# Performance work log

Measured on AMD Instinct MI355X. Metric: run time of the kernel, lower is better.

## Reference

```python
import jax, jax.numpy as jnp
import numpy as np

B, A, F, C = 32, 64, 128, 128


def _mlp(h, W0, b0, W1, b1):
    # LinearLayer stack: Linear(2F->C) + ReLU, Linear(C->C) + ReLU
    h = jax.nn.relu(h @ W0 + b0)
    h = jax.nn.relu(h @ W1 + b1)
    return h


def setup_inputs() -> dict:
    key = jax.random.key(0)
    k0, k1, k2 = jax.random.split(key, 3)
    x = jax.random.normal(k0, (B, A, F), dtype=jnp.float32)
    W0 = jax.random.normal(k1, (2 * F, C), dtype=jnp.float32) * (1.0 / np.sqrt(2 * F))
    b0 = jnp.zeros((C,), dtype=jnp.float32)
    W1 = jax.random.normal(k2, (C, C), dtype=jnp.float32) * (1.0 / np.sqrt(C))
    b1 = jnp.zeros((C,), dtype=jnp.float32)
    return {"x": x, "W0": W0, "b0": b0, "W1": W1, "b1": b1}


def reference(x, W0, b0, W1, b1):
    nb, na, nf = x.shape
    # atom_tile[b,i,j]   = x[b,i]  (first atom of the pair)
    # atom_repeat[b,i,j] = x[b,j]  (second atom of the pair)
    xi = jnp.broadcast_to(x[:, :, None, :], (nb, na, na, nf))
    xj = jnp.broadcast_to(x[:, None, :, :], (nb, na, na, nf))
    # pair_x0 = cat(atom_tile, atom_repeat) = [x_i, x_j]
    p0 = jnp.concatenate([xi, xj], axis=-1).reshape(nb * na * na, 2 * nf)
    # pair_x1 = cat(atom_repeat, atom_tile) = [x_j, x_i]
    p1 = jnp.concatenate([xj, xi], axis=-1).reshape(nb * na * na, 2 * nf)
    h0 = _mlp(p0, W0, b0, W1, b1).reshape(nb, na * na, -1)
    h1 = _mlp(p1, W0, b0, W1, b1).reshape(nb, na * na, -1)
    return h0 + h1
```

## Files before the change

kernel.cpp:

```cpp
#include <hip/hip_runtime.h>
#include <hip/hip_bf16.h>

typedef float  f32x4  __attribute__((ext_vector_type(4)));
typedef __bf16 bf16x8 __attribute__((ext_vector_type(8)));
typedef unsigned int   u32x4 __attribute__((ext_vector_type(4)));
typedef unsigned short u16x4 __attribute__((ext_vector_type(4)));

#define NB 32
#define NA 64
#define NF 128
#define NC 128

__global__ __launch_bounds__(512) void prep_kernel(
    const float* __restrict__ x, const float* __restrict__ W0,
    const float* __restrict__ b0, const float* __restrict__ W1,
    float* __restrict__ u, float* __restrict__ v,
    unsigned short* __restrict__ w1t)
{
    int blk = blockIdx.x;
    int tid = threadIdx.x;
    if (blk < 256) {
        __shared__ __align__(16) float xs[8 * 128];
        int b = blk >> 3;
        int g = blk & 7;
        if (tid < 256)
            ((f32x4*)xs)[tid] =
                ((const f32x4*)(x + (size_t)(b * NA + g * 8) * NF))[tid];
        __syncthreads();
        int c = tid & 127;
        int h = (tid >> 7) & 1;
        int s = tid >> 8;
        const float* wp = W0 + (size_t)h * 128 * NC + c;
        const float* xp = xs + s * 4 * 128;
        float a0 = 0.f, a1 = 0.f, a2 = 0.f, a3 = 0.f;
        #pragma unroll 8
        for (int f = 0; f < 128; ++f) {
            float w = wp[(size_t)f * NC];
            a0 = fmaf(xp[f],       w, a0);
            a1 = fmaf(xp[128 + f], w, a1);
            a2 = fmaf(xp[256 + f], w, a2);
            a3 = fmaf(xp[384 + f], w, a3);
        }
        int row = b * NA + g * 8 + s * 4;
        if (h == 0) {
            u[(size_t)(row + 0) * NC + c] = a0;
            u[(size_t)(row + 1) * NC + c] = a1;
            u[(size_t)(row + 2) * NC + c] = a2;
            u[(size_t)(row + 3) * NC + c] = a3;
        } else {
            float bb = b0[c];
            v[(size_t)(row + 0) * NC + c] = a0 + bb;
            v[(size_t)(row + 1) * NC + c] = a1 + bb;
            v[(size_t)(row + 2) * NC + c] = a2 + bb;
            v[(size_t)(row + 3) * NC + c] = a3 + bb;
        }
    } else {
        int t = (blk - 256) * 512 + tid;
        int n = t >> 5;
        int k = (t & 31) * 4;
        u16x4 o;
        #pragma unroll
        for (int e = 0; e < 4; ++e) {
            float w = W1[(size_t)(k + e) * NC + n];
            o[e] = __builtin_bit_cast(unsigned short, (__bf16)w);
        }
        *(u16x4*)(w1t + (size_t)n * NC + k) = o;
    }
}

__device__ inline bf16x8 relu_cvt_bf16(f32x4 a, f32x4 b)
{
    bf16x8 r;
    #pragma unroll
    for (int e = 0; e < 4; ++e) {
        r[e]     = (__bf16)fmaxf(a[e], 0.f);
        r[e + 4] = (__bf16)fmaxf(b[e], 0.f);
    }
    return r;
}

__global__ __launch_bounds__(256, 3) void pair_mlp_kernel(
    const float* __restrict__ b1g, const float* __restrict__ u,
    const float* __restrict__ v, const unsigned short* __restrict__ w1t,
    float* __restrict__ out)
{
    __shared__ __align__(16) float          u_s[16 * 128];
    __shared__ __align__(16) float          v_s[16 * 128];
    __shared__ __align__(16) unsigned short w_s[128 * 128];

    int blk = blockIdx.x;
    int b = blk / 36;
    int t = blk % 36;
    int I = 0;
    while (t >= 8 - I) { t -= 8 - I; ++I; }
    int J = I + t;

    int tid = threadIdx.x;

    #pragma unroll
    for (int p = 0; p < 4; ++p) {
        int idx = p * 256 + tid;
        int arr = idx >> 9;
        int rem = idx & 511;
        int row = rem >> 5;
        int c   = rem & 31;
        int ga  = b * NA + ((row < 8) ? (I * 8 + row) : (J * 8 + (row & 7)));
        const float* src = (arr ? v : u) + (size_t)ga * NC;
        float*       dst = (arr ? v_s : u_s) + row * 128;
        int sc = (c & 24) | ((c ^ row) & 7);
        ((f32x4*)dst)[sc] = ((const f32x4*)src)[c];
    }
    #pragma unroll
    for (int p = 0; p < 8; ++p) {
        int idx = p * 256 + tid;
        int n = idx >> 4;
        int c = idx & 15;
        int sc = c ^ (n & 7);
        ((u32x4*)(w_s + n * 128))[sc] = ((const u32x4*)(w1t + (size_t)n * NC))[c];
    }
    __syncthreads();

    int wave = tid >> 6;
    int lane = tid & 63;
    int llo  = lane & 15;
    int lhi  = lane >> 4;
    int r    = wave * 16 + llo;
    int il   = r >> 3;
    int jl   = r & 7;

    f32x4 acc0[8], acc1[8];
    f32x4 z = {0.f, 0.f, 0.f, 0.f};
    #pragma unroll
    for (int nf = 0; nf < 8; ++nf) { acc0[nf] = z; acc1[nf] = z; }

    const float* uI = u_s + il * 128;
    const float* vI = v_s + il * 128;
    const float* uJ = u_s + (8 + jl) * 128;
    const float* vJ = v_s + (8 + jl) * 128;

    #pragma unroll
    for (int kk = 0; kk < 4; ++kk) {
        int kc  = kk * 8 + lhi * 2;
        int kc1 = kc + 1;
        int sA0 = (kc  & 24) | ((kc  ^ il) & 7);
        int sA1 = (kc1 & 24) | ((kc1 ^ il) & 7);
        int sB0 = (kc  & 24) | ((kc  ^ jl) & 7);
        int sB1 = (kc1 & 24) | ((kc1 ^ jl) & 7);

        f32x4 uIa = ((const f32x4*)uI)[sA0];
        f32x4 uIb = ((const f32x4*)uI)[sA1];
        f32x4 vIa = ((const f32x4*)vI)[sA0];
        f32x4 vIb = ((const f32x4*)vI)[sA1];
        f32x4 uJa = ((const f32x4*)uJ)[sB0];
        f32x4 uJb = ((const f32x4*)uJ)[sB1];
        f32x4 vJa = ((const f32x4*)vJ)[sB0];
        f32x4 vJb = ((const f32x4*)vJ)[sB1];

        bf16x8 h0 = relu_cvt_bf16(uIa + vJa, uIb + vJb);
        bf16x8 h1 = relu_cvt_bf16(uJa + vIa, uJb + vIb);

        int kcw = kk * 4 + lhi;
        int scW = kcw ^ (llo & 7);
        #pragma unroll
        for (int nf = 0; nf < 8; ++nf) {
            bf16x8 wf = ((const bf16x8*)(w_s + (nf * 16 + llo) * 128))[scW];
            acc0[nf] = __builtin_amdgcn_mfma_f32_16x16x32_bf16(wf, h0, acc0[nf], 0, 0, 0);
            acc1[nf] = __builtin_amdgcn_mfma_f32_16x16x32_bf16(wf, h1, acc1[nf], 0, 0, 0);
        }
    }

    int Ig = I * 8 + il;
    int Jg = J * 8 + jl;
    float* p1 = out + ((size_t)b * 4096 + Ig * 64 + Jg) * 128 + lhi * 4;
    float* p2 = out + ((size_t)b * 4096 + Jg * 64 + Ig) * 128 + lhi * 4;
    bool mirror = (I != J);
    #pragma unroll
    for (int nf = 0; nf < 8; ++nf) {
        f32x4 bias = *(const f32x4*)(b1g + nf * 16 + lhi * 4);
        f32x4 val;
        #pragma unroll
        for (int e = 0; e < 4; ++e)
            val[e] = fmaxf(acc0[nf][e] + bias[e], 0.f) +
                     fmaxf(acc1[nf][e] + bias[e], 0.f);
        *(f32x4*)(p1 + nf * 16) = val;
        if (mirror)
            *(f32x4*)(p2 + nf * 16) = val;
    }
}

extern "C" void kernel_launch(void* const* d_in, const int* in_sizes, int n_in,
                              void* d_out, int out_size, void* d_ws, size_t ws_size,
                              hipStream_t stream)
{
    (void)in_sizes; (void)n_in; (void)out_size; (void)ws_size;
    const float* x  = (const float*)d_in[0];
    const float* W0 = (const float*)d_in[1];
    const float* b0 = (const float*)d_in[2];
    const float* W1 = (const float*)d_in[3];
    const float* b1 = (const float*)d_in[4];
    float* out = (float*)d_out;

    float* u = (float*)d_ws;
    float* v = u + (size_t)NB * NA * NC;
    unsigned short* w1t = (unsigned short*)(v + (size_t)NB * NA * NC);

    prep_kernel<<<264, 512, 0, stream>>>(x, W0, b0, W1, u, v, w1t);
    pair_mlp_kernel<<<32 * 36, 256, 0, stream>>>(b1, u, v, w1t, out);
}
```

Baseline: 31.56 us.

## Pre-pack W1 into MFMA fragment order and load it directly from global memory

After: 43.99 us. +39.4%, slower.

```diff
diff --git a/kernel.cpp b/kernel.cpp
--- a/kernel.cpp
+++ b/kernel.cpp
@@ -15,7 +15,7 @@
     const float* __restrict__ x, const float* __restrict__ W0,
     const float* __restrict__ b0, const float* __restrict__ W1,
     float* __restrict__ u, float* __restrict__ v,
-    unsigned short* __restrict__ w1t)
+    unsigned short* __restrict__ wfrag)
 {
     int blk = blockIdx.x;
     int tid = threadIdx.x;
@@ -55,16 +55,23 @@
             v[(size_t)(row + 3) * NC + c] = a3 + bb;
         }
     } else {
-        int t = (blk - 256) * 512 + tid;
-        int n = t >> 5;
-        int k = (t & 31) * 4;
+        int idx  = ((blk - 256) * 512 + tid) * 4;
+        int e0   = idx & 7;
+        int lane = (idx >> 3) & 63;
+        int frag = idx >> 9;
+        int kk   = frag >> 3;
+        int nf   = frag & 7;
+        int llo  = lane & 15;
+        int lhi  = lane >> 4;
+        int n    = nf * 16 + llo;
+        int kb   = kk * 32 + lhi * 8 + e0;
         u16x4 o;
         #pragma unroll
         for (int e = 0; e < 4; ++e) {
-            float w = W1[(size_t)(k + e) * NC + n];
+            float w = W1[(size_t)(kb + e) * NC + n];
             o[e] = __builtin_bit_cast(unsigned short, (__bf16)w);
         }
-        *(u16x4*)(w1t + (size_t)n * NC + k) = o;
+        *(u16x4*)(wfrag + idx) = o;
     }
 }
 
@@ -79,14 +86,13 @@
     return r;
 }
 
-__global__ __launch_bounds__(256, 3) void pair_mlp_kernel(
+__global__ __launch_bounds__(256, 4) void pair_mlp_kernel(
     const float* __restrict__ b1g, const float* __restrict__ u,
-    const float* __restrict__ v, const unsigned short* __restrict__ w1t,
+    const float* __restrict__ v, const unsigned short* __restrict__ wfrag,
     float* __restrict__ out)
 {
-    __shared__ __align__(16) float          u_s[16 * 128];
-    __shared__ __align__(16) float          v_s[16 * 128];
-    __shared__ __align__(16) unsigned short w_s[128 * 128];
+    __shared__ __align__(16) float u_s[16 * 128];
+    __shared__ __align__(16) float v_s[16 * 128];
 
     int blk = blockIdx.x;
     int b = blk / 36;
@@ -110,14 +116,6 @@
         int sc = (c & 24) | ((c ^ row) & 7);
         ((f32x4*)dst)[sc] = ((const f32x4*)src)[c];
     }
-    #pragma unroll
-    for (int p = 0; p < 8; ++p) {
-        int idx = p * 256 + tid;
-        int n = idx >> 4;
-        int c = idx & 15;
-        int sc = c ^ (n & 7);
-        ((u32x4*)(w_s + n * 128))[sc] = ((const u32x4*)(w1t + (size_t)n * NC))[c];
-    }
     __syncthreads();
 
     int wave = tid >> 6;
@@ -137,6 +135,7 @@
     const float* vI = v_s + il * 128;
     const float* uJ = u_s + (8 + jl) * 128;
     const float* vJ = v_s + (8 + jl) * 128;
+    const bf16x8* wf = (const bf16x8*)wfrag;
 
     #pragma unroll
     for (int kk = 0; kk < 4; ++kk) {
@@ -159,13 +158,11 @@
         bf16x8 h0 = relu_cvt_bf16(uIa + vJa, uIb + vJb);
         bf16x8 h1 = relu_cvt_bf16(uJa + vIa, uJb + vIb);
 
-        int kcw = kk * 4 + lhi;
-        int scW = kcw ^ (llo & 7);
         #pragma unroll
         for (int nf = 0; nf < 8; ++nf) {
-            bf16x8 wf = ((const bf16x8*)(w_s + (nf * 16 + llo) * 128))[scW];
-            acc0[nf] = __builtin_amdgcn_mfma_f32_16x16x32_bf16(wf, h0, acc0[nf], 0, 0, 0);
-            acc1[nf] = __builtin_amdgcn_mfma_f32_16x16x32_bf16(wf, h1, acc1[nf], 0, 0, 0);
+            bf16x8 w = wf[(kk * 8 + nf) * 64 + lane];
+            acc0[nf] = __builtin_amdgcn_mfma_f32_16x16x32_bf16(w, h0, acc0[nf], 0, 0, 0);
+            acc1[nf] = __builtin_amdgcn_mfma_f32_16x16x32_bf16(w, h1, acc1[nf], 0, 0, 0);
         }
     }
 
@@ -202,8 +199,8 @@
 
     float* u = (float*)d_ws;
     float* v = u + (size_t)NB * NA * NC;
-    unsigned short* w1t = (unsigned short*)(v + (size_t)NB * NA * NC);
-
-    prep_kernel<<<264, 512, 0, stream>>>(x, W0, b0, W1, u, v, w1t);
-    pair_mlp_kernel<<<32 * 36, 256, 0, stream>>>(b1, u, v, w1t, out);
-}
+    unsigned short* wfrag = (unsigned short*)(v + (size_t)NB * NA * NC);
+
+    prep_kernel<<<264, 512, 0, stream>>>(x, W0, b0, W1, u, v, wfrag);
+    pair_mlp_kernel<<<32 * 36, 256, 0, stream>>>(b1, u, v, wfrag, out);
+}
```

## Fuse first-layer projection into pair MLP kernel with register-resident W1 fragments

Applied to the files above, without the earlier changes.

After: 34.96 us. +10.8%, slower.

```diff
diff --git a/kernel.cpp b/kernel.cpp
--- a/kernel.cpp
+++ b/kernel.cpp
@@ -12,60 +12,44 @@
 #define NC 128
 
 __global__ __launch_bounds__(512) void prep_kernel(
-    const float* __restrict__ x, const float* __restrict__ W0,
-    const float* __restrict__ b0, const float* __restrict__ W1,
-    float* __restrict__ u, float* __restrict__ v,
-    unsigned short* __restrict__ w1t)
-{
-    int blk = blockIdx.x;
-    int tid = threadIdx.x;
-    if (blk < 256) {
-        __shared__ __align__(16) float xs[8 * 128];
-        int b = blk >> 3;
-        int g = blk & 7;
-        if (tid < 256)
-            ((f32x4*)xs)[tid] =
-                ((const f32x4*)(x + (size_t)(b * NA + g * 8) * NF))[tid];
-        __syncthreads();
-        int c = tid & 127;
-        int h = (tid >> 7) & 1;
-        int s = tid >> 8;
-        const float* wp = W0 + (size_t)h * 128 * NC + c;
-        const float* xp = xs + s * 4 * 128;
-        float a0 = 0.f, a1 = 0.f, a2 = 0.f, a3 = 0.f;
-        #pragma unroll 8
-        for (int f = 0; f < 128; ++f) {
-            float w = wp[(size_t)f * NC];
-            a0 = fmaf(xp[f],       w, a0);
-            a1 = fmaf(xp[128 + f], w, a1);
-            a2 = fmaf(xp[256 + f], w, a2);
-            a3 = fmaf(xp[384 + f], w, a3);
-        }
-        int row = b * NA + g * 8 + s * 4;
-        if (h == 0) {
-            u[(size_t)(row + 0) * NC + c] = a0;
-            u[(size_t)(row + 1) * NC + c] = a1;
-            u[(size_t)(row + 2) * NC + c] = a2;
-            u[(size_t)(row + 3) * NC + c] = a3;
-        } else {
-            float bb = b0[c];
-            v[(size_t)(row + 0) * NC + c] = a0 + bb;
-            v[(size_t)(row + 1) * NC + c] = a1 + bb;
-            v[(size_t)(row + 2) * NC + c] = a2 + bb;
-            v[(size_t)(row + 3) * NC + c] = a3 + bb;
-        }
+    const float* __restrict__ W0, const float* __restrict__ W1,
+    unsigned short* __restrict__ w0t, unsigned short* __restrict__ w1f)
+{
+    int blk = blockIdx.x, tid = threadIdx.x;
+    if (blk < 16) {
+        int idx = (blk * 512 + tid) * 4;
+        int c  = idx >> 8;
+        int kb = idx & 255;
+        u16x4 o;
+        #pragma unroll
+        for (int e = 0; e < 4; ++e)
+            o[e] = __builtin_bit_cast(unsigned short,
+                     (__bf16)W0[(size_t)(kb + e) * NC + c]);
+        *(u16x4*)(w0t + idx) = o;
     } else {
-        int t = (blk - 256) * 512 + tid;
-        int n = t >> 5;
-        int k = (t & 31) * 4;
+        int idx = ((blk - 16) * 512 + tid) * 4;
+        int e0   = idx & 7;
+        int fl   = idx >> 3;
+        int lane = fl & 63;
+        int frag = fl >> 6;
+        int kk = frag >> 3, nf = frag & 7;
+        int k = kk * 32 + (lane >> 4) * 8 + e0;
+        int n = nf * 16 + (lane & 15);
         u16x4 o;
         #pragma unroll
-        for (int e = 0; e < 4; ++e) {
-            float w = W1[(size_t)(k + e) * NC + n];
-            o[e] = __builtin_bit_cast(unsigned short, (__bf16)w);
-        }
-        *(u16x4*)(w1t + (size_t)n * NC + k) = o;
-    }
+        for (int e = 0; e < 4; ++e)
+            o[e] = __builtin_bit_cast(unsigned short,
+                     (__bf16)W1[(size_t)(k + e) * NC + n]);
+        *(u16x4*)(w1f + idx) = o;
+    }
+}
+
+__device__ inline bf16x8 cvt2_bf16(f32x4 a, f32x4 b)
+{
+    bf16x8 r;
+    #pragma unroll
+    for (int e = 0; e < 4; ++e) { r[e] = (__bf16)a[e]; r[e + 4] = (__bf16)b[e]; }
+    return r;
 }
 
 __device__ inline bf16x8 relu_cvt_bf16(f32x4 a, f32x4 b)
@@ -79,112 +63,154 @@
     return r;
 }
 
-__global__ __launch_bounds__(256, 3) void pair_mlp_kernel(
-    const float* __restrict__ b1g, const float* __restrict__ u,
-    const float* __restrict__ v, const unsigned short* __restrict__ w1t,
-    float* __restrict__ out)
-{
-    __shared__ __align__(16) float          u_s[16 * 128];
-    __shared__ __align__(16) float          v_s[16 * 128];
-    __shared__ __align__(16) unsigned short w_s[128 * 128];
+__global__ __launch_bounds__(512, 1) void fused_kernel(
+    const float* __restrict__ x, const float* __restrict__ b0g,
+    const float* __restrict__ b1g, const unsigned short* __restrict__ w0t,
+    const unsigned short* __restrict__ w1f, float* __restrict__ out)
+{
+    __shared__ __align__(16) unsigned short w0_s[128 * 256];
+    __shared__ __align__(16) float          u_s[64 * 128];
+    __shared__ __align__(16) float          v_s[64 * 128];
 
     int blk = blockIdx.x;
-    int b = blk / 36;
-    int t = blk % 36;
-    int I = 0;
-    while (t >= 8 - I) { t -= 8 - I; ++I; }
-    int J = I + t;
-
-    int tid = threadIdx.x;
-
-    #pragma unroll
-    for (int p = 0; p < 4; ++p) {
-        int idx = p * 256 + tid;
-        int arr = idx >> 9;
-        int rem = idx & 511;
-        int row = rem >> 5;
-        int c   = rem & 31;
-        int ga  = b * NA + ((row < 8) ? (I * 8 + row) : (J * 8 + (row & 7)));
-        const float* src = (arr ? v : u) + (size_t)ga * NC;
-        float*       dst = (arr ? v_s : u_s) + row * 128;
-        int sc = (c & 24) | ((c ^ row) & 7);
-        ((f32x4*)dst)[sc] = ((const f32x4*)src)[c];
-    }
+    int b = blk >> 3;
+    int g = blk & 7;
+    int tid  = threadIdx.x;
+    int wave = tid >> 6, lane = tid & 63;
+    int llo  = lane & 15, lhi = lane >> 4;
+
+    bf16x8 wreg[4][8];
+    #pragma unroll
+    for (int kk = 0; kk < 4; ++kk)
+        #pragma unroll
+        for (int nf = 0; nf < 8; ++nf)
+            wreg[kk][nf] = ((const bf16x8*)w1f)[(kk * 8 + nf) * 64 + lane];
+
+    int uv = wave >> 2, Mt = wave & 3;
+    const float* xrow = x + ((size_t)b * NA + Mt * 16 + llo) * NF;
+    f32x4 xa[4][2];
+    #pragma unroll
+    for (int kk = 0; kk < 4; ++kk) {
+        xa[kk][0] = *(const f32x4*)(xrow + kk * 32 + lhi * 8);
+        xa[kk][1] = *(const f32x4*)(xrow + kk * 32 + lhi * 8 + 4);
+    }
+    float bias0[8];
+    #pragma unroll
+    for (int nt = 0; nt < 8; ++nt) bias0[nt] = b0g[nt * 16 + llo];
+
     #pragma unroll
     for (int p = 0; p < 8; ++p) {
-        int idx = p * 256 + tid;
-        int n = idx >> 4;
-        int c = idx & 15;
-        int sc = c ^ (n & 7);
-        ((u32x4*)(w_s + n * 128))[sc] = ((const u32x4*)(w1t + (size_t)n * NC))[c];
+        int chunk = p * 512 + tid;
+        int c  = chunk >> 5;
+        int kc = chunk & 31;
+        int sc = (kc & 24) | ((kc ^ c) & 7);
+        ((u32x4*)(w0_s + c * 256))[sc] = ((const u32x4*)(w0t + c * 256))[kc];
     }
     __syncthreads();
 
-    int wave = tid >> 6;
-    int lane = tid & 63;
-    int llo  = lane & 15;
-    int lhi  = lane >> 4;
-    int r    = wave * 16 + llo;
-    int il   = r >> 3;
-    int jl   = r & 7;
-
-    f32x4 acc0[8], acc1[8];
+    f32x4 acc[8];
     f32x4 z = {0.f, 0.f, 0.f, 0.f};
     #pragma unroll
-    for (int nf = 0; nf < 8; ++nf) { acc0[nf] = z; acc1[nf] = z; }
-
-    const float* uI = u_s + il * 128;
-    const float* vI = v_s + il * 128;
-    const float* uJ = u_s + (8 + jl) * 128;
-    const float* vJ = v_s + (8 + jl) * 128;
-
+    for (int nt = 0; nt < 8; ++nt) acc[nt] = z;
     #pragma unroll
     for (int kk = 0; kk < 4; ++kk) {
-        int kc  = kk * 8 + lhi * 2;
-        int kc1 = kc + 1;
-        int sA0 = (kc  & 24) | ((kc  ^ il) & 7);
-        int sA1 = (kc1 & 24) | ((kc1 ^ il) & 7);
-        int sB0 = (kc  & 24) | ((kc  ^ jl) & 7);
-        int sB1 = (kc1 & 24) | ((kc1 ^ jl) & 7);
-
-        f32x4 uIa = ((const f32x4*)uI)[sA0];
-        f32x4 uIb = ((const f32x4*)uI)[sA1];
-        f32x4 vIa = ((const f32x4*)vI)[sA0];
-        f32x4 vIb = ((const f32x4*)vI)[sA1];
-        f32x4 uJa = ((const f32x4*)uJ)[sB0];
-        f32x4 uJb = ((const f32x4*)uJ)[sB1];
-        f32x4 vJa = ((const f32x4*)vJ)[sB0];
-        f32x4 vJb = ((const f32x4*)vJ)[sB1];
-
-        bf16x8 h0 = relu_cvt_bf16(uIa + vJa, uIb + vJb);
-        bf16x8 h1 = relu_cvt_bf16(uJa + vIa, uJb + vIb);
-
-        int kcw = kk * 4 + lhi;
-        int scW = kcw ^ (llo & 7);
+        bf16x8 af = cvt2_bf16(xa[kk][0], xa[kk][1]);
+        int kcb = uv * 16 + kk * 4 + lhi;
+        #pragma unroll
+        for (int nt = 0; nt < 8; ++nt) {
+            int c  = nt * 16 + llo;
+            int sc = (kcb & 24) | ((kcb ^ c) & 7);
+            bf16x8 bf = ((const bf16x8*)(w0_s + c * 256))[sc];
+            acc[nt] = __builtin_amdgcn_mfma_f32_16x16x32_bf16(af, bf, acc[nt], 0, 0, 0);
+        }
+    }
+    {
+        float* dst = uv ? v_s : u_s;
+        #pragma unroll
+        for (int nt = 0; nt < 8; ++nt) {
+            f32x4 a = acc[nt];
+            if (uv) {
+                #pragma unroll
+                for (int e = 0; e < 4; ++e) a[e] += bias0[nt];
+            }
+            int c  = nt * 16 + llo;
+            int kc = c >> 2;
+            #pragma unroll
+            for (int q = 0; q < 4; ++q) {
+                int atom = Mt * 16 + lhi * 4 + q;
+                int sc = (kc & 24) | ((kc ^ atom) & 7);
+                dst[atom * 128 + sc * 4 + (c & 3)] = a[q];
+            }
+        }
+    }
+    __syncthreads();
+
+    for (int s = wave; s < 18; s += 8) {
+        int tg = g * 18 + s;
+        int t  = tg >> 2;
+        int q  = tg & 3;
+        int I = 0, tr = t;
+        while (tr >= 8 - I) { tr -= 8 - I; ++I; }
+        int J = I + tr;
+
+        int r  = q * 16 + llo;
+        int il = r >> 3, jl = r & 7;
+        int rowI = I * 8 + il;
+        int rowJ = J * 8 + jl;
+        const float* uI = u_s + rowI * 128;
+        const float* vI = v_s + rowI * 128;
+        const float* uJ = u_s + rowJ * 128;
+        const float* vJ = v_s + rowJ * 128;
+
+        f32x4 acc0[8], acc1[8];
+        #pragma unroll
+        for (int nf = 0; nf < 8; ++nf) { acc0[nf] = z; acc1[nf] = z; }
+
+        #pragma unroll
+        for (int kk = 0; kk < 4; ++kk) {
+            int kc  = kk * 8 + lhi * 2;
+            int kc1 = kc + 1;
+            int sA0 = (kc  & 24) | ((kc  ^ rowI) & 7);
+            int sA1 = (kc1 & 24) | ((kc1 ^ rowI) & 7);
+            int sB0 = (kc  & 24) | ((kc  ^ rowJ) & 7);
+            int sB1 = (kc1 & 24) | ((kc1 ^ rowJ) & 7);
+
+            f32x4 uIa = ((const f32x4*)uI)[sA0];
+            f32x4 uIb = ((const f32x4*)uI)[sA1];
+            f32x4 vIa = ((const f32x4*)vI)[sA0];
+            f32x4 vIb = ((const f32x4*)vI)[sA1];
+            f32x4 uJa = ((const f32x4*)uJ)[sB0];
+            f32x4 uJb = ((const f32x4*)uJ)[sB1];
+            f32x4 vJa = ((const f32x4*)vJ)[sB0];
+            f32x4 vJb = ((const f32x4*)vJ)[sB1];
+
+            bf16x8 h0 = relu_cvt_bf16(uIa + vJa, uIb + vJb);
+            bf16x8 h1 = relu_cvt_bf16(uJa + vIa, uJb + vIb);
+
+            #pragma unroll
+            for (int nf = 0; nf < 8; ++nf) {
+                acc0[nf] = __builtin_amdgcn_mfma_f32_16x16x32_bf16(
+                    wreg[kk][nf], h0, acc0[nf], 0, 0, 0);
+                acc1[nf] = __builtin_amdgcn_mfma_f32_16x16x32_bf16(
+                    wreg[kk][nf], h1, acc1[nf], 0, 0, 0);
+            }
+        }
+
+        float* p1 = out + ((size_t)b * 4096 + rowI * 64 + rowJ) * 128 + lhi * 4;
+        float* p2 = out + ((size_t)b * 4096 + rowJ * 64 + rowI) * 128 + lhi * 4;
+        bool mirror = (I != J);
         #pragma unroll
         for (int nf = 0; nf < 8; ++nf) {
-            bf16x8 wf = ((const bf16x8*)(w_s + (nf * 16 + llo) * 128))[scW];
-            acc0[nf] = __builtin_amdgcn_mfma_f32_16x16x32_bf16(wf, h0, acc0[nf], 0, 0, 0);
-            acc1[nf] = __builtin_amdgcn_mfma_f32_16x16x32_bf16(wf, h1, acc1[nf], 0, 0, 0);
-        }
-    }
-
-    int Ig = I * 8 + il;
-    int Jg = J * 8 + jl;
-    float* p1 = out + ((size_t)b * 4096 + Ig * 64 + Jg) * 128 + lhi * 4;
-    float* p2 = out + ((size_t)b * 4096 + Jg * 64 + Ig) * 128 + lhi * 4;
-    bool mirror = (I != J);
-    #pragma unroll
-    for (int nf = 0; nf < 8; ++nf) {
-        f32x4 bias = *(const f32x4*)(b1g + nf * 16 + lhi * 4);
-        f32x4 val;
-        #pragma unroll
-        for (int e = 0; e < 4; ++e)
-            val[e] = fmaxf(acc0[nf][e] + bias[e], 0.f) +
-                     fmaxf(acc1[nf][e] + bias[e], 0.f);
-        *(f32x4*)(p1 + nf * 16) = val;
-        if (mirror)
-            *(f32x4*)(p2 + nf * 16) = val;
+            f32x4 bias = *(const f32x4*)(b1g + nf * 16 + lhi * 4);
+            f32x4 val;
+            #pragma unroll
+            for (int e = 0; e < 4; ++e)
+                val[e] = fmaxf(acc0[nf][e] + bias[e], 0.f) +
+                         fmaxf(acc1[nf][e] + bias[e], 0.f);
+            *(f32x4*)(p1 + nf * 16) = val;
+            if (mirror)
+                *(f32x4*)(p2 + nf * 16) = val;
+        }
     }
 }
 
@@ -200,10 +226,9 @@
     const float* b1 = (const float*)d_in[4];
     float* out = (float*)d_out;
 
-    float* u = (float*)d_ws;
-    float* v = u + (size_t)NB * NA * NC;
-    unsigned short* w1t = (unsigned short*)(v + (size_t)NB * NA * NC);
-
-    prep_kernel<<<264, 512, 0, stream>>>(x, W0, b0, W1, u, v, w1t);
-    pair_mlp_kernel<<<32 * 36, 256, 0, stream>>>(b1, u, v, w1t, out);
-}
+    unsigned short* w0t = (unsigned short*)d_ws;
+    unsigned short* w1f = w0t + 128 * 256;
+
+    prep_kernel<<<24, 512, 0, stream>>>(W0, W1, w0t, w1f);
+    fused_kernel<<<NB * 8, 512, 0, stream>>>(x, b0, b1, w0t, w1f, out);
+}
```
